# Performance work log

Hardware: AMD Instinct MI355X
Metric: run time of the kernel (lower is better)

Reference implementation:

```python
import jax, jax.numpy as jnp
import numpy as np

EMBED = 1024
HEADS = 16
HEAD_DIM = EMBED // HEADS


def setup_inputs() -> dict:
    key = jax.random.key(0)
    ks = jax.random.split(key, 8)
    B, S = 2, 2048
    value = jax.random.normal(ks[0], (B, S, EMBED), dtype=jnp.float32)
    key_t = jax.random.normal(ks[1], (B, S, EMBED), dtype=jnp.float32)
    query = jax.random.normal(ks[2], (B, S, EMBED), dtype=jnp.float32)
    scale = 1.0 / np.sqrt(EMBED)
    Wv = jax.random.normal(ks[3], (EMBED, EMBED), dtype=jnp.float32) * scale
    Wk = jax.random.normal(ks[4], (EMBED, EMBED), dtype=jnp.float32) * scale
    Wq = jax.random.normal(ks[5], (EMBED, EMBED), dtype=jnp.float32) * scale
    Wo = jax.random.normal(ks[6], (EMBED, EMBED), dtype=jnp.float32) * scale
    bo = jax.random.normal(ks[7], (EMBED,), dtype=jnp.float32) * 0.01
    return {"value": value, "key": key_t, "query": query,
            "Wv": Wv, "Wk": Wk, "Wq": Wq, "Wo": Wo, "bo": bo}


def reference(value, key, query, Wv, Wk, Wq, Wo, bo):
    B = query.shape[0]
    # Linear (torch: y = x @ W.T), then split heads -> [B, H, S, D]
    def split(x, W):
        y = jnp.einsum('bse,fe->bsf', x, W)
        return y.reshape(B, -1, HEADS, HEAD_DIM).transpose(0, 2, 1, 3)
    v = split(value, Wv)
    k = split(key, Wk)
    q = split(query, Wq)
    scores = jnp.einsum('bhqd,bhkd->bhqk', q, k) / jnp.sqrt(jnp.float32(HEAD_DIM))
    attn = jax.nn.softmax(scores, axis=-1)
    out = jnp.einsum('bhqk,bhkd->bhqd', attn, v)
    out = out.transpose(0, 2, 1, 3).reshape(B, -1, EMBED)
    return jnp.einsum('bse,fe->bsf', out, Wo) + bo
```

## Files before the change

kernel.cpp:

```cpp
#include <hip/hip_runtime.h>


#define SEQ   2048
#define EMB   1024
#define NHEAD 16
#define HDIM  64
#define NTOK  4096

typedef __attribute__((ext_vector_type(8))) __bf16 bf16x8;
typedef __attribute__((ext_vector_type(4))) float  f32x4;

#define OFF_XV  0u
#define OFF_XK  4194304u
#define OFF_XQ  8388608u
#define OFF_WV  12582912u
#define OFF_WK  13631488u
#define OFF_WQ  14680064u
#define OFF_WO  15728640u
#define OFF_VB  16777216u
#define OFF_KB  20971520u
#define OFF_QB  25165824u
#define OFF_VT  4194304u
#define OFF_ATT 0u

typedef __attribute__((address_space(1))) void g_void;
typedef __attribute__((address_space(3))) void l_void;

__device__ __forceinline__ void async_cp16(const void* g, void* l) {
  __builtin_amdgcn_global_load_lds((g_void*)(void*)g, (l_void*)l, 16, 0, 0);
}

__device__ __forceinline__ unsigned short f2bf(float f) {
  __bf16 h = (__bf16)f;
  return __builtin_bit_cast(unsigned short, h);
}

__device__ __forceinline__ f32x4 mfma16(bf16x8 a, bf16x8 b, f32x4 c) {
  return __builtin_amdgcn_mfma_f32_16x16x32_bf16(a, b, c, 0, 0, 0);
}

__global__ __launch_bounds__(256) void cvt_bf16(
    const float* __restrict__ s0, const float* __restrict__ s1,
    const float* __restrict__ s2, const float* __restrict__ s3,
    const float* __restrict__ s4, const float* __restrict__ s5,
    const float* __restrict__ s6, unsigned short* __restrict__ ws)
{
  int t = blockIdx.y;
  const float* s; unsigned off; int n8;
  switch (t) {
    case 0:  s = s0; off = OFF_XV; n8 = 524288; break;
    case 1:  s = s1; off = OFF_XK; n8 = 524288; break;
    case 2:  s = s2; off = OFF_XQ; n8 = 524288; break;
    case 3:  s = s3; off = OFF_WV; n8 = 131072; break;
    case 4:  s = s4; off = OFF_WK; n8 = 131072; break;
    case 5:  s = s5; off = OFF_WQ; n8 = 131072; break;
    default: s = s6; off = OFF_WO; n8 = 131072; break;
  }
  const float4* sf = (const float4*)s;
  unsigned short* d = ws + off;
  for (int i = blockIdx.x * 256 + threadIdx.x; i < n8; i += gridDim.x * 256) {
    float4 a = sf[2 * i], b = sf[2 * i + 1];
    uint4 o;
    o.x = (unsigned)f2bf(a.x) | ((unsigned)f2bf(a.y) << 16);
    o.y = (unsigned)f2bf(a.z) | ((unsigned)f2bf(a.w) << 16);
    o.z = (unsigned)f2bf(b.x) | ((unsigned)f2bf(b.y) << 16);
    o.w = (unsigned)f2bf(b.z) | ((unsigned)f2bf(b.w) << 16);
    *(uint4*)&d[(size_t)i * 8] = o;
  }
}

__global__ __launch_bounds__(256) void gemm_bf16(
    unsigned short* __restrict__ ws, float* __restrict__ dout,
    const float* __restrict__ bo, int mode_base)
{
  int mode = mode_base + blockIdx.z;
  const unsigned short* A;
  const unsigned short* W;
  if (mode == 0)      { A = ws + OFF_XV;  W = ws + OFF_WV; }
  else if (mode == 1) { A = ws + OFF_XK;  W = ws + OFF_WK; }
  else if (mode == 2) { A = ws + OFF_XQ;  W = ws + OFF_WQ; }
  else                { A = ws + OFF_ATT; W = ws + OFF_WO; }

  int tid = threadIdx.x;
  int lane = tid & 63;
  int wid = tid >> 6;
  int l15 = lane & 15, lg = lane >> 4;
  int wm = wid >> 1, wn = wid & 1;
  int m0 = blockIdx.y * 128, n0 = blockIdx.x * 128;
  int c0 = wid * 2;

  __shared__ unsigned short Ab[2][4096];
  __shared__ unsigned short Bb[2][4096];

  f32x4 acc[4][4];
#pragma unroll
  for (int i = 0; i < 4; ++i)
#pragma unroll
    for (int j = 0; j < 4; ++j) acc[i][j] = (f32x4)0.0f;

#pragma unroll
  for (int i = 0; i < 2; ++i) {
    int c = (c0 + i) * 64 + lane;
    int row = c >> 2, cs = c & 3;
    int sc = (cs ^ ((row >> 1) & 3)) * 8;
    async_cp16(A + (size_t)(m0 + row) * 1024 + sc, &Ab[0][(c0 + i) * 512]);
    async_cp16(W + (size_t)(n0 + row) * 1024 + sc, &Bb[0][(c0 + i) * 512]);
  }
  __syncthreads();

  for (int kt = 0; kt < 32; ++kt) {
    int cur = kt & 1;
    if (kt < 31) {
      int k0 = (kt + 1) * 32;
#pragma unroll
      for (int i = 0; i < 2; ++i) {
        int c = (c0 + i) * 64 + lane;
        int row = c >> 2, cs = c & 3;
        int sc = (cs ^ ((row >> 1) & 3)) * 8;
        async_cp16(A + (size_t)(m0 + row) * 1024 + k0 + sc, &Ab[cur ^ 1][(c0 + i) * 512]);
        async_cp16(W + (size_t)(n0 + row) * 1024 + k0 + sc, &Bb[cur ^ 1][(c0 + i) * 512]);
      }
    }
    bf16x8 af[4], bfr[4];
#pragma unroll
    for (int mf = 0; mf < 4; ++mf) {
      int ar = wm * 64 + mf * 16 + l15;
      af[mf] = *(const bf16x8*)&Ab[cur][ar * 32 + (lg ^ ((ar >> 1) & 3)) * 8];
    }
#pragma unroll
    for (int nf = 0; nf < 4; ++nf) {
      int br = wn * 64 + nf * 16 + l15;
      bfr[nf] = *(const bf16x8*)&Bb[cur][br * 32 + (lg ^ ((br >> 1) & 3)) * 8];
    }
#pragma unroll
    for (int mf = 0; mf < 4; ++mf)
#pragma unroll
      for (int nf = 0; nf < 4; ++nf)
        acc[mf][nf] = mfma16(af[mf], bfr[nf], acc[mf][nf]);
    __syncthreads();
  }

  if (mode < 3) {
    unsigned short* outp = ws + OFF_VB + (unsigned)mode * 4194304u;
    float scale = (mode == 2) ? 0.18033688011112042f : 1.0f;
#pragma unroll
    for (int mf = 0; mf < 4; ++mf)
#pragma unroll
      for (int nf = 0; nf < 4; ++nf)
#pragma unroll
        for (int r = 0; r < 4; ++r) {
          int token = m0 + wm * 64 + mf * 16 + lg * 4 + r;
          int col   = n0 + wn * 64 + nf * 16 + l15;
          size_t o = (((size_t)(token >> 11) * NHEAD + (col >> 6)) * SEQ
                      + (token & 2047)) * HDIM + (col & 63);
          outp[o] = f2bf(acc[mf][nf][r] * scale);
        }
  } else {
#pragma unroll
    for (int nf = 0; nf < 4; ++nf) {
      int col = n0 + wn * 64 + nf * 16 + l15;
      float bias = bo[col];
#pragma unroll
      for (int mf = 0; mf < 4; ++mf)
#pragma unroll
        for (int r = 0; r < 4; ++r) {
          int token = m0 + wm * 64 + mf * 16 + lg * 4 + r;
          dout[(size_t)token * EMB + col] = acc[mf][nf][r] + bias;
        }
    }
  }
}

__global__ __launch_bounds__(256) void vtrans(
    const unsigned short* __restrict__ vsrc, unsigned short* __restrict__ vdst)
{
  __shared__ unsigned short T[64][72];
  int tid = threadIdx.x;
  int bh = blockIdx.y;
  int s0 = blockIdx.x * 64;
  const unsigned short* v = vsrc + (size_t)bh * SEQ * HDIM;
  unsigned short* o = vdst + (size_t)bh * HDIM * SEQ;

  int r = tid >> 2, cq = tid & 3;
  const uint4* src = (const uint4*)&v[(size_t)(s0 + r) * HDIM + cq * 16];
  uint4 d0 = src[0], d1 = src[1];
  *(uint4*)&T[r][cq * 16]     = d0;
  *(uint4*)&T[r][cq * 16 + 8] = d1;
  __syncthreads();

  int d = tid >> 2, sc = tid & 3;
  uint4 t4[2];
  unsigned short* tmp = (unsigned short*)t4;
#pragma unroll
  for (int j = 0; j < 16; ++j) tmp[j] = T[sc * 16 + j][d];
  *(uint4*)&o[(size_t)d * SEQ + s0 + sc * 16]     = t4[0];
  *(uint4*)&o[(size_t)d * SEQ + s0 + sc * 16 + 8] = t4[1];
}

__global__ __launch_bounds__(256) void attn_fwd(unsigned short* __restrict__ ws)
{
  int tid = threadIdx.x, lane = tid & 63, wid = tid >> 6;
  int l15 = lane & 15, lg = lane >> 4;
  int bh = blockIdx.x & 31;
  int q0 = (blockIdx.x >> 5) * 128;

  const unsigned short* qb = ws + OFF_QB + (size_t)bh * SEQ * HDIM;
  const unsigned short* kb = ws + OFF_KB + (size_t)bh * SEQ * HDIM;
  const unsigned short* vt = ws + OFF_VT + (size_t)bh * HDIM * SEQ;
  unsigned short* att = ws + OFF_ATT;

  __shared__ unsigned short Kb[2][4096];
  __shared__ unsigned short Vb[2][4096];
  __shared__ unsigned short Pb[4][2304];

  bf16x8 qf[2][2];
#pragma unroll
  for (int mf = 0; mf < 2; ++mf)
#pragma unroll
    for (int kk = 0; kk < 2; ++kk)
      qf[mf][kk] = *(const bf16x8*)
          &qb[(size_t)(q0 + wid * 32 + mf * 16 + l15) * HDIM + kk * 32 + lg * 8];

  f32x4 O[2][4];
#pragma unroll
  for (int mf = 0; mf < 2; ++mf)
#pragma unroll
    for (int nf = 0; nf < 4; ++nf) O[mf][nf] = (f32x4)0.0f;
  float mrow[2][4], lp[2][4];
#pragma unroll
  for (int mf = 0; mf < 2; ++mf)
#pragma unroll
    for (int r = 0; r < 4; ++r) { mrow[mf][r] = -1e30f; lp[mf][r] = 0.0f; }

  int c0 = wid * 2;
  auto stage = [&](int buf, int kv0) {
#pragma unroll
    for (int i = 0; i < 2; ++i) {
      int c = (c0 + i) * 64 + lane;
      int row = c >> 3, cs = c & 7;
      int scol = (cs ^ (row & 7)) * 8;
      async_cp16(kb + (size_t)(kv0 + row) * HDIM + scol, &Kb[buf][(c0 + i) * 512]);
      async_cp16(vt + (size_t)row * SEQ + kv0 + scol,     &Vb[buf][(c0 + i) * 512]);
    }
  };

  stage(0, 0);
  __syncthreads();

  for (int it = 0; it < 32; ++it) {
    int cur = it & 1;
    if (it < 31) stage(cur ^ 1, (it + 1) * 64);

    f32x4 S[2][4];
#pragma unroll
    for (int mf = 0; mf < 2; ++mf)
#pragma unroll
      for (int nf = 0; nf < 4; ++nf) S[mf][nf] = (f32x4)0.0f;
#pragma unroll
    for (int kk = 0; kk < 2; ++kk) {
#pragma unroll
      for (int nf = 0; nf < 4; ++nf) {
        int row = nf * 16 + l15;
        int off = (row * 128 + kk * 64 + lg * 16) ^ ((row & 7) << 4);
        bf16x8 kf = *(const bf16x8*)((const char*)&Kb[cur][0] + off);
        S[0][nf] = mfma16(qf[0][kk], kf, S[0][nf]);
        S[1][nf] = mfma16(qf[1][kk], kf, S[1][nf]);
      }
    }

    float lmax[2][4];
    bool need = false;
#pragma unroll
    for (int mf = 0; mf < 2; ++mf)
#pragma unroll
      for (int r = 0; r < 4; ++r) {
        float rx = fmaxf(fmaxf(S[mf][0][r], S[mf][1][r]),
                         fmaxf(S[mf][2][r], S[mf][3][r]));
        lmax[mf][r] = rx;
        need = need || (rx > mrow[mf][r] + 8.0f);
      }
    if (__any((int)need)) {
#pragma unroll
      for (int mf = 0; mf < 2; ++mf)
#pragma unroll
        for (int r = 0; r < 4; ++r) {
          float rx = lmax[mf][r];
          rx = fmaxf(rx, __shfl_xor(rx, 1));
          rx = fmaxf(rx, __shfl_xor(rx, 2));
          rx = fmaxf(rx, __shfl_xor(rx, 4));
          rx = fmaxf(rx, __shfl_xor(rx, 8));
          float mold = mrow[mf][r];
          float mnew = fmaxf(mold, rx);
          float scl = __builtin_amdgcn_exp2f(mold - mnew);
          mrow[mf][r] = mnew;
          lp[mf][r] *= scl;
#pragma unroll
          for (int nf = 0; nf < 4; ++nf) O[mf][nf][r] *= scl;
        }
    }
#pragma unroll
    for (int mf = 0; mf < 2; ++mf)
#pragma unroll
      for (int r = 0; r < 4; ++r) {
        float m = mrow[mf][r];
        float s0 = __builtin_amdgcn_exp2f(S[mf][0][r] - m);
        float s1 = __builtin_amdgcn_exp2f(S[mf][1][r] - m);
        float s2 = __builtin_amdgcn_exp2f(S[mf][2][r] - m);
        float s3 = __builtin_amdgcn_exp2f(S[mf][3][r] - m);
        S[mf][0][r] = s0; S[mf][1][r] = s1; S[mf][2][r] = s2; S[mf][3][r] = s3;
        lp[mf][r] += (s0 + s1) + (s2 + s3);
      }

    unsigned short* pw = &Pb[wid][0];
#pragma unroll
    for (int mf = 0; mf < 2; ++mf)
#pragma unroll
      for (int nf = 0; nf < 4; ++nf)
#pragma unroll
        for (int r = 0; r < 4; ++r)
          pw[(mf * 16 + lg * 4 + r) * 72 + nf * 16 + l15] = f2bf(S[mf][nf][r]);

#pragma unroll
    for (int kk = 0; kk < 2; ++kk) {
      bf16x8 pf[2];
      pf[0] = *(const bf16x8*)&pw[(l15) * 72 + kk * 32 + lg * 8];
      pf[1] = *(const bf16x8*)&pw[(16 + l15) * 72 + kk * 32 + lg * 8];
#pragma unroll
      for (int nf = 0; nf < 4; ++nf) {
        int d = nf * 16 + l15;
        int off = (d * 128 + kk * 64 + lg * 16) ^ ((d & 7) << 4);
        bf16x8 vf = *(const bf16x8*)((const char*)&Vb[cur][0] + off);
        O[0][nf] = mfma16(pf[0], vf, O[0][nf]);
        O[1][nf] = mfma16(pf[1], vf, O[1][nf]);
      }
    }
    __syncthreads();
  }

  int b = bh >> 4, h = bh & 15;
#pragma unroll
  for (int mf = 0; mf < 2; ++mf)
#pragma unroll
    for (int r = 0; r < 4; ++r) {
      float ps = lp[mf][r];
      ps += __shfl_xor(ps, 1);
      ps += __shfl_xor(ps, 2);
      ps += __shfl_xor(ps, 4);
      ps += __shfl_xor(ps, 8);
      float inv = 1.0f / ps;
      int srow = q0 + wid * 32 + mf * 16 + lg * 4 + r;
#pragma unroll
      for (int nf = 0; nf < 4; ++nf) {
        int e = h * 64 + nf * 16 + l15;
        att[((size_t)b * SEQ + srow) * EMB + e] = f2bf(O[mf][nf][r] * inv);
      }
    }
}

extern "C" void kernel_launch(void* const* d_in, const int* in_sizes, int n_in,
                              void* d_out, int out_size, void* d_ws, size_t ws_size,
                              hipStream_t stream)
{
  const float* value = (const float*)d_in[0];
  const float* key_t = (const float*)d_in[1];
  const float* query = (const float*)d_in[2];
  const float* Wv = (const float*)d_in[3];
  const float* Wk = (const float*)d_in[4];
  const float* Wq = (const float*)d_in[5];
  const float* Wo = (const float*)d_in[6];
  const float* bo = (const float*)d_in[7];
  unsigned short* ws = (unsigned short*)d_ws;
  float* out = (float*)d_out;

  cvt_bf16<<<dim3(512, 7), 256, 0, stream>>>(value, key_t, query, Wv, Wk, Wq, Wo, ws);
  gemm_bf16<<<dim3(8, 32, 3), 256, 0, stream>>>(ws, out, bo, 0);
  vtrans<<<dim3(32, 32), 256, 0, stream>>>(ws + OFF_VB, ws + OFF_VT);
  attn_fwd<<<512, 256, 0, stream>>>(ws);
  gemm_bf16<<<dim3(8, 32, 1), 256, 0, stream>>>(ws, out, bo, 3);
}
```

Measured before the change: 263.2 us.

## Halve attention query tile per block, swizzle P buffer, add MFMA priority hints

The attention kernel now handles 64 query rows per block (16 per wave) instead of 128 and launches twice as many blocks, which cuts registers per wave and should raise occupancy and spread work across more CUs. The P staging buffer in LDS now uses an XOR-swizzled 64-wide layout instead of a padded 72-wide one, and s_setprio raises wave priority around the MFMA sections. The cost is that each K/V tile loaded into LDS is reused by half as many query rows, which doubles K/V global and LDS traffic per output row.

New measurement: 278.9 us. +6.0%, slower.

```diff
diff --git a/kernel.cpp b/kernel.cpp
--- a/kernel.cpp
+++ b/kernel.cpp
@@ -202,7 +202,7 @@
   int tid = threadIdx.x, lane = tid & 63, wid = tid >> 6;
   int l15 = lane & 15, lg = lane >> 4;
   int bh = blockIdx.x & 31;
-  int q0 = (blockIdx.x >> 5) * 128;
+  int q0 = (blockIdx.x >> 5) * 64;
 
   const unsigned short* qb = ws + OFF_QB + (size_t)bh * SEQ * HDIM;
   const unsigned short* kb = ws + OFF_KB + (size_t)bh * SEQ * HDIM;
@@ -211,26 +211,20 @@
 
   __shared__ unsigned short Kb[2][4096];
   __shared__ unsigned short Vb[2][4096];
-  __shared__ unsigned short Pb[4][2304];
-
-  bf16x8 qf[2][2];
-#pragma unroll
-  for (int mf = 0; mf < 2; ++mf)
-#pragma unroll
-    for (int kk = 0; kk < 2; ++kk)
-      qf[mf][kk] = *(const bf16x8*)
-          &qb[(size_t)(q0 + wid * 32 + mf * 16 + l15) * HDIM + kk * 32 + lg * 8];
-
-  f32x4 O[2][4];
-#pragma unroll
-  for (int mf = 0; mf < 2; ++mf)
-#pragma unroll
-    for (int nf = 0; nf < 4; ++nf) O[mf][nf] = (f32x4)0.0f;
-  float mrow[2][4], lp[2][4];
-#pragma unroll
-  for (int mf = 0; mf < 2; ++mf)
-#pragma unroll
-    for (int r = 0; r < 4; ++r) { mrow[mf][r] = -1e30f; lp[mf][r] = 0.0f; }
+  __shared__ unsigned short Pb[4][1024];
+
+  bf16x8 qf[2];
+#pragma unroll
+  for (int kk = 0; kk < 2; ++kk)
+    qf[kk] = *(const bf16x8*)
+        &qb[(size_t)(q0 + wid * 16 + l15) * HDIM + kk * 32 + lg * 8];
+
+  f32x4 O[4];
+#pragma unroll
+  for (int nf = 0; nf < 4; ++nf) O[nf] = (f32x4)0.0f;
+  float mrow[4], lp[4];
+#pragma unroll
+  for (int r = 0; r < 4; ++r) { mrow[r] = -1e30f; lp[r] = 0.0f; }
 
   int c0 = wid * 2;
   auto stage = [&](int buf, int kv0) {
@@ -251,11 +245,10 @@
     int cur = it & 1;
     if (it < 31) stage(cur ^ 1, (it + 1) * 64);
 
-    f32x4 S[2][4];
-#pragma unroll
-    for (int mf = 0; mf < 2; ++mf)
-#pragma unroll
-      for (int nf = 0; nf < 4; ++nf) S[mf][nf] = (f32x4)0.0f;
+    f32x4 S[4];
+#pragma unroll
+    for (int nf = 0; nf < 4; ++nf) S[nf] = (f32x4)0.0f;
+    __builtin_amdgcn_s_setprio(1);
 #pragma unroll
     for (int kk = 0; kk < 2; ++kk) {
 #pragma unroll
@@ -263,98 +256,90 @@
         int row = nf * 16 + l15;
         int off = (row * 128 + kk * 64 + lg * 16) ^ ((row & 7) << 4);
         bf16x8 kf = *(const bf16x8*)((const char*)&Kb[cur][0] + off);
-        S[0][nf] = mfma16(qf[0][kk], kf, S[0][nf]);
-        S[1][nf] = mfma16(qf[1][kk], kf, S[1][nf]);
-      }
-    }
-
-    float lmax[2][4];
+        S[nf] = mfma16(qf[kk], kf, S[nf]);
+      }
+    }
+    __builtin_amdgcn_s_setprio(0);
+
+    float lmax[4];
     bool need = false;
 #pragma unroll
-    for (int mf = 0; mf < 2; ++mf)
+    for (int r = 0; r < 4; ++r) {
+      float rx = fmaxf(fmaxf(S[0][r], S[1][r]), fmaxf(S[2][r], S[3][r]));
+      lmax[r] = rx;
+      need = need || (rx > mrow[r] + 8.0f);
+    }
+    if (__any((int)need)) {
 #pragma unroll
       for (int r = 0; r < 4; ++r) {
-        float rx = fmaxf(fmaxf(S[mf][0][r], S[mf][1][r]),
-                         fmaxf(S[mf][2][r], S[mf][3][r]));
-        lmax[mf][r] = rx;
-        need = need || (rx > mrow[mf][r] + 8.0f);
-      }
-    if (__any((int)need)) {
-#pragma unroll
-      for (int mf = 0; mf < 2; ++mf)
-#pragma unroll
-        for (int r = 0; r < 4; ++r) {
-          float rx = lmax[mf][r];
-          rx = fmaxf(rx, __shfl_xor(rx, 1));
-          rx = fmaxf(rx, __shfl_xor(rx, 2));
-          rx = fmaxf(rx, __shfl_xor(rx, 4));
-          rx = fmaxf(rx, __shfl_xor(rx, 8));
-          float mold = mrow[mf][r];
-          float mnew = fmaxf(mold, rx);
-          float scl = __builtin_amdgcn_exp2f(mold - mnew);
-          mrow[mf][r] = mnew;
-          lp[mf][r] *= scl;
-#pragma unroll
-          for (int nf = 0; nf < 4; ++nf) O[mf][nf][r] *= scl;
-        }
-    }
-#pragma unroll
-    for (int mf = 0; mf < 2; ++mf)
+        float rx = lmax[r];
+        rx = fmaxf(rx, __shfl_xor(rx, 1));
+        rx = fmaxf(rx, __shfl_xor(rx, 2));
+        rx = fmaxf(rx, __shfl_xor(rx, 4));
+        rx = fmaxf(rx, __shfl_xor(rx, 8));
+        float mold = mrow[r];
+        float mnew = fmaxf(mold, rx);
+        float scl = __builtin_amdgcn_exp2f(mold - mnew);
+        mrow[r] = mnew;
+        lp[r] *= scl;
+#pragma unroll
+        for (int nf = 0; nf < 4; ++nf) O[nf][r] *= scl;
+      }
+    }
+#pragma unroll
+    for (int r = 0; r < 4; ++r) {
+      float m = mrow[r];
+      float s0 = __builtin_amdgcn_exp2f(S[0][r] - m);
+      float s1 = __builtin_amdgcn_exp2f(S[1][r] - m);
+      float s2 = __builtin_amdgcn_exp2f(S[2][r] - m);
+      float s3 = __builtin_amdgcn_exp2f(S[3][r] - m);
+      S[0][r] = s0; S[1][r] = s1; S[2][r] = s2; S[3][r] = s3;
+      lp[r] += (s0 + s1) + (s2 + s3);
+    }
+
+    unsigned short* pw = &Pb[wid][0];
+#pragma unroll
+    for (int nf = 0; nf < 4; ++nf)
 #pragma unroll
       for (int r = 0; r < 4; ++r) {
-        float m = mrow[mf][r];
-        float s0 = __builtin_amdgcn_exp2f(S[mf][0][r] - m);
-        float s1 = __builtin_amdgcn_exp2f(S[mf][1][r] - m);
-        float s2 = __builtin_amdgcn_exp2f(S[mf][2][r] - m);
-        float s3 = __builtin_amdgcn_exp2f(S[mf][3][r] - m);
-        S[mf][0][r] = s0; S[mf][1][r] = s1; S[mf][2][r] = s2; S[mf][3][r] = s3;
-        lp[mf][r] += (s0 + s1) + (s2 + s3);
-      }
-
-    unsigned short* pw = &Pb[wid][0];
-#pragma unroll
-    for (int mf = 0; mf < 2; ++mf)
-#pragma unroll
-      for (int nf = 0; nf < 4; ++nf)
-#pragma unroll
-        for (int r = 0; r < 4; ++r)
-          pw[(mf * 16 + lg * 4 + r) * 72 + nf * 16 + l15] = f2bf(S[mf][nf][r]);
-
+        int m = lg * 4 + r;
+        int chunk = (nf * 2 + (l15 >> 3)) ^ (m & 7);
+        pw[m * 64 + chunk * 8 + (l15 & 7)] = f2bf(S[nf][r]);
+      }
+
+    __builtin_amdgcn_s_setprio(1);
 #pragma unroll
     for (int kk = 0; kk < 2; ++kk) {
-      bf16x8 pf[2];
-      pf[0] = *(const bf16x8*)&pw[(l15) * 72 + kk * 32 + lg * 8];
-      pf[1] = *(const bf16x8*)&pw[(16 + l15) * 72 + kk * 32 + lg * 8];
+      int chunk = (kk * 4 + lg) ^ (l15 & 7);
+      bf16x8 pf = *(const bf16x8*)&pw[l15 * 64 + chunk * 8];
 #pragma unroll
       for (int nf = 0; nf < 4; ++nf) {
         int d = nf * 16 + l15;
         int off = (d * 128 + kk * 64 + lg * 16) ^ ((d & 7) << 4);
         bf16x8 vf = *(const bf16x8*)((const char*)&Vb[cur][0] + off);
-        O[0][nf] = mfma16(pf[0], vf, O[0][nf]);
-        O[1][nf] = mfma16(pf[1], vf, O[1][nf]);
-      }
-    }
+        O[nf] = mfma16(pf, vf, O[nf]);
+      }
+    }
+    __builtin_amdgcn_s_setprio(0);
     __syncthreads();
   }
 
   int b = bh >> 4, h = bh & 15;
 #pragma unroll
-  for (int mf = 0; mf < 2; ++mf)
-#pragma unroll
-    for (int r = 0; r < 4; ++r) {
-      float ps = lp[mf][r];
-      ps += __shfl_xor(ps, 1);
-      ps += __shfl_xor(ps, 2);
-      ps += __shfl_xor(ps, 4);
-      ps += __shfl_xor(ps, 8);
-      float inv = 1.0f / ps;
-      int srow = q0 + wid * 32 + mf * 16 + lg * 4 + r;
-#pragma unroll
-      for (int nf = 0; nf < 4; ++nf) {
-        int e = h * 64 + nf * 16 + l15;
-        att[((size_t)b * SEQ + srow) * EMB + e] = f2bf(O[mf][nf][r] * inv);
-      }
-    }
+  for (int r = 0; r < 4; ++r) {
+    float ps = lp[r];
+    ps += __shfl_xor(ps, 1);
+    ps += __shfl_xor(ps, 2);
+    ps += __shfl_xor(ps, 4);
+    ps += __shfl_xor(ps, 8);
+    float inv = 1.0f / ps;
+    int srow = q0 + wid * 16 + lg * 4 + r;
+#pragma unroll
+    for (int nf = 0; nf < 4; ++nf) {
+      int e = h * 64 + nf * 16 + l15;
+      att[((size_t)b * SEQ + srow) * EMB + e] = f2bf(O[nf][r] * inv);
+    }
+  }
 }
 
 extern "C" void kernel_launch(void* const* d_in, const int* in_sizes, int n_in,
@@ -375,6 +360,6 @@
   cvt_bf16<<<dim3(512, 7), 256, 0, stream>>>(value, key_t, query, Wv, Wk, Wq, Wo, ws);
   gemm_bf16<<<dim3(8, 32, 3), 256, 0, stream>>>(ws, out, bo, 0);
   vtrans<<<dim3(32, 32), 256, 0, stream>>>(ws + OFF_VB, ws + OFF_VT);
-  attn_fwd<<<512, 256, 0, stream>>>(ws);
+  attn_fwd<<<1024, 256, 0, stream>>>(ws);
   gemm_bf16<<<dim3(8, 32, 1), 256, 0, stream>>>(ws, out, bo, 3);
 }
```

## Fuse V transpose into projection GEMM and keep attention P in registers

Applied to the files above, without the earlier changes.

The projection GEMM epilogue now stages results through shared memory and writes coalesced 16-byte stores. For V it writes the transposed [d, s] layout directly, which removes the separate vtrans kernel and its extra pass over V. The attention kernel computes S transposed (K as the A operand, with a permuted K row order) so each lane holds a full query row. This lets P be packed into bf16 MFMA operands in registers without an LDS round-trip, and it simplifies the row max and sum reductions. s_setprio hints are also added around the MFMA blocks; the main risk is the correctness of the permutation and layout mapping.

Result: faster. 219.8 us (-16.5%).

```diff
diff --git a/kernel.cpp b/kernel.cpp
--- a/kernel.cpp
+++ b/kernel.cpp
@@ -17,10 +17,9 @@
 #define OFF_WK  13631488u
 #define OFF_WQ  14680064u
 #define OFF_WO  15728640u
-#define OFF_VB  16777216u
+#define OFF_VT  16777216u
 #define OFF_KB  20971520u
 #define OFF_QB  25165824u
-#define OFF_VT  4194304u
 #define OFF_ATT 0u
 
 typedef __attribute__((address_space(1))) void g_void;
@@ -89,8 +88,9 @@
   int m0 = blockIdx.y * 128, n0 = blockIdx.x * 128;
   int c0 = wid * 2;
 
-  __shared__ unsigned short Ab[2][4096];
-  __shared__ unsigned short Bb[2][4096];
+  __shared__ unsigned short SM[16384];
+  unsigned short (*Ab)[4096] = (unsigned short(*)[4096])SM;
+  unsigned short (*Bb)[4096] = (unsigned short(*)[4096])(SM + 8192);
 
   f32x4 acc[4][4];
 #pragma unroll
@@ -132,16 +132,40 @@
       int br = wn * 64 + nf * 16 + l15;
       bfr[nf] = *(const bf16x8*)&Bb[cur][br * 32 + (lg ^ ((br >> 1) & 3)) * 8];
     }
+    __builtin_amdgcn_s_setprio(1);
 #pragma unroll
     for (int mf = 0; mf < 4; ++mf)
 #pragma unroll
       for (int nf = 0; nf < 4; ++nf)
         acc[mf][nf] = mfma16(af[mf], bfr[nf], acc[mf][nf]);
+    __builtin_amdgcn_s_setprio(0);
     __syncthreads();
   }
 
-  if (mode < 3) {
-    unsigned short* outp = ws + OFF_VB + (unsigned)mode * 4194304u;
+  if (mode == 0) {
+#pragma unroll
+    for (int mf = 0; mf < 4; ++mf)
+#pragma unroll
+      for (int nf = 0; nf < 4; ++nf)
+#pragma unroll
+        for (int r = 0; r < 4; ++r) {
+          int c = wn * 64 + nf * 16 + l15;
+          int s = wm * 64 + mf * 16 + lg * 4 + r;
+          SM[c * 128 + (s ^ ((c & 7) << 3))] = f2bf(acc[mf][nf][r]);
+        }
+    __syncthreads();
+    int sidx = tid & 15, cbase = tid >> 4;
+    size_t b = (size_t)(m0 >> 11);
+#pragma unroll
+    for (int i = 0; i < 8; ++i) {
+      int c = i * 16 + cbase;
+      int h = (n0 >> 6) + (c >> 6);
+      uint4 v = *(const uint4*)&SM[c * 128 + ((sidx ^ (c & 7)) * 8)];
+      size_t bh = b * NHEAD + h;
+      *(uint4*)&ws[OFF_VT + (bh * HDIM + (c & 63)) * SEQ + (m0 & 2047) + sidx * 8] = v;
+    }
+  } else if (mode < 3) {
+    unsigned short* outp = ws + ((mode == 1) ? OFF_KB : OFF_QB);
     float scale = (mode == 2) ? 0.18033688011112042f : 1.0f;
 #pragma unroll
     for (int mf = 0; mf < 4; ++mf)
@@ -149,12 +173,22 @@
       for (int nf = 0; nf < 4; ++nf)
 #pragma unroll
         for (int r = 0; r < 4; ++r) {
-          int token = m0 + wm * 64 + mf * 16 + lg * 4 + r;
-          int col   = n0 + wn * 64 + nf * 16 + l15;
-          size_t o = (((size_t)(token >> 11) * NHEAD + (col >> 6)) * SEQ
-                      + (token & 2047)) * HDIM + (col & 63);
-          outp[o] = f2bf(acc[mf][nf][r] * scale);
-        }
+          int s = wm * 64 + mf * 16 + lg * 4 + r;
+          int c = wn * 64 + nf * 16 + l15;
+          SM[s * 128 + (c ^ ((s & 7) << 3))] = f2bf(acc[mf][nf][r] * scale);
+        }
+    __syncthreads();
+    int l = tid & 15, rb = tid >> 4;
+    int half = l >> 3, j = l & 7;
+    size_t b = (size_t)(m0 >> 11);
+#pragma unroll
+    for (int i = 0; i < 8; ++i) {
+      int s = i * 16 + rb;
+      uint4 v = *(const uint4*)&SM[s * 128 + half * 64 + ((j ^ (s & 7)) * 8)];
+      int h = (n0 >> 6) + half;
+      size_t bh = b * NHEAD + h;
+      *(uint4*)&outp[(bh * SEQ + ((m0 + s) & 2047)) * HDIM + j * 8] = v;
+    }
   } else {
 #pragma unroll
     for (int nf = 0; nf < 4; ++nf) {
@@ -169,32 +203,6 @@
         }
     }
   }
-}
-
-__global__ __launch_bounds__(256) void vtrans(
-    const unsigned short* __restrict__ vsrc, unsigned short* __restrict__ vdst)
-{
-  __shared__ unsigned short T[64][72];
-  int tid = threadIdx.x;
-  int bh = blockIdx.y;
-  int s0 = blockIdx.x * 64;
-  const unsigned short* v = vsrc + (size_t)bh * SEQ * HDIM;
-  unsigned short* o = vdst + (size_t)bh * HDIM * SEQ;
-
-  int r = tid >> 2, cq = tid & 3;
-  const uint4* src = (const uint4*)&v[(size_t)(s0 + r) * HDIM + cq * 16];
-  uint4 d0 = src[0], d1 = src[1];
-  *(uint4*)&T[r][cq * 16]     = d0;
-  *(uint4*)&T[r][cq * 16 + 8] = d1;
-  __syncthreads();
-
-  int d = tid >> 2, sc = tid & 3;
-  uint4 t4[2];
-  unsigned short* tmp = (unsigned short*)t4;
-#pragma unroll
-  for (int j = 0; j < 16; ++j) tmp[j] = T[sc * 16 + j][d];
-  *(uint4*)&o[(size_t)d * SEQ + s0 + sc * 16]     = t4[0];
-  *(uint4*)&o[(size_t)d * SEQ + s0 + sc * 16 + 8] = t4[1];
 }
 
 __global__ __launch_bounds__(256) void attn_fwd(unsigned short* __restrict__ ws)
@@ -211,7 +219,6 @@
 
   __shared__ unsigned short Kb[2][4096];
   __shared__ unsigned short Vb[2][4096];
-  __shared__ unsigned short Pb[4][2304];
 
   bf16x8 qf[2][2];
 #pragma unroll
@@ -226,21 +233,20 @@
   for (int mf = 0; mf < 2; ++mf)
 #pragma unroll
     for (int nf = 0; nf < 4; ++nf) O[mf][nf] = (f32x4)0.0f;
-  float mrow[2][4], lp[2][4];
-#pragma unroll
-  for (int mf = 0; mf < 2; ++mf)
-#pragma unroll
-    for (int r = 0; r < 4; ++r) { mrow[mf][r] = -1e30f; lp[mf][r] = 0.0f; }
+  float mrow[2], lp[2];
+#pragma unroll
+  for (int mf = 0; mf < 2; ++mf) { mrow[mf] = -1e30f; lp[mf] = 0.0f; }
 
   int c0 = wid * 2;
   auto stage = [&](int buf, int kv0) {
 #pragma unroll
     for (int i = 0; i < 2; ++i) {
       int c = (c0 + i) * 64 + lane;
-      int row = c >> 3, cs = c & 7;
-      int scol = (cs ^ (row & 7)) * 8;
-      async_cp16(kb + (size_t)(kv0 + row) * HDIM + scol, &Kb[buf][(c0 + i) * 512]);
-      async_cp16(vt + (size_t)row * SEQ + kv0 + scol,     &Vb[buf][(c0 + i) * 512]);
+      int p = c >> 3, cs = c & 7;
+      int scol = (cs ^ (p & 7)) * 8;
+      int kpi = ((p >> 4) & 1) * 32 + ((p >> 2) & 3) * 8 + (p >> 5) * 4 + (p & 3);
+      async_cp16(kb + (size_t)(kv0 + kpi) * HDIM + scol, &Kb[buf][(c0 + i) * 512]);
+      async_cp16(vt + (size_t)p * SEQ + kv0 + scol,       &Vb[buf][(c0 + i) * 512]);
     }
   };
 
@@ -256,98 +262,107 @@
     for (int mf = 0; mf < 2; ++mf)
 #pragma unroll
       for (int nf = 0; nf < 4; ++nf) S[mf][nf] = (f32x4)0.0f;
+    __builtin_amdgcn_s_setprio(1);
 #pragma unroll
     for (int kk = 0; kk < 2; ++kk) {
 #pragma unroll
       for (int nf = 0; nf < 4; ++nf) {
-        int row = nf * 16 + l15;
-        int off = (row * 128 + kk * 64 + lg * 16) ^ ((row & 7) << 4);
+        int p = nf * 16 + l15;
+        int off = (p * 128 + kk * 64 + lg * 16) ^ ((p & 7) << 4);
         bf16x8 kf = *(const bf16x8*)((const char*)&Kb[cur][0] + off);
-        S[0][nf] = mfma16(qf[0][kk], kf, S[0][nf]);
-        S[1][nf] = mfma16(qf[1][kk], kf, S[1][nf]);
-      }
-    }
-
-    float lmax[2][4];
+        S[0][nf] = mfma16(kf, qf[0][kk], S[0][nf]);
+        S[1][nf] = mfma16(kf, qf[1][kk], S[1][nf]);
+      }
+    }
+    __builtin_amdgcn_s_setprio(0);
+
+    float lmax[2];
     bool need = false;
 #pragma unroll
-    for (int mf = 0; mf < 2; ++mf)
-#pragma unroll
-      for (int r = 0; r < 4; ++r) {
-        float rx = fmaxf(fmaxf(S[mf][0][r], S[mf][1][r]),
-                         fmaxf(S[mf][2][r], S[mf][3][r]));
-        lmax[mf][r] = rx;
-        need = need || (rx > mrow[mf][r] + 8.0f);
-      }
+    for (int mf = 0; mf < 2; ++mf) {
+      float rx = S[mf][0][0];
+#pragma unroll
+      for (int nf = 0; nf < 4; ++nf)
+#pragma unroll
+        for (int r = 0; r < 4; ++r) rx = fmaxf(rx, S[mf][nf][r]);
+      lmax[mf] = rx;
+      need = need || (rx > mrow[mf] + 8.0f);
+    }
     if (__any((int)need)) {
+      float scl[2];
+#pragma unroll
+      for (int mf = 0; mf < 2; ++mf) {
+        float rx = lmax[mf];
+        rx = fmaxf(rx, __shfl_xor(rx, 16));
+        rx = fmaxf(rx, __shfl_xor(rx, 32));
+        float mold = mrow[mf];
+        float mnew = fmaxf(mold, rx);
+        scl[mf] = __builtin_amdgcn_exp2f(mold - mnew);
+        mrow[mf] = mnew;
+        lp[mf] *= scl[mf];
+      }
 #pragma unroll
       for (int mf = 0; mf < 2; ++mf)
 #pragma unroll
         for (int r = 0; r < 4; ++r) {
-          float rx = lmax[mf][r];
-          rx = fmaxf(rx, __shfl_xor(rx, 1));
-          rx = fmaxf(rx, __shfl_xor(rx, 2));
-          rx = fmaxf(rx, __shfl_xor(rx, 4));
-          rx = fmaxf(rx, __shfl_xor(rx, 8));
-          float mold = mrow[mf][r];
-          float mnew = fmaxf(mold, rx);
-          float scl = __builtin_amdgcn_exp2f(mold - mnew);
-          mrow[mf][r] = mnew;
-          lp[mf][r] *= scl;
-#pragma unroll
-          for (int nf = 0; nf < 4; ++nf) O[mf][nf][r] *= scl;
-        }
-    }
-#pragma unroll
-    for (int mf = 0; mf < 2; ++mf)
-#pragma unroll
-      for (int r = 0; r < 4; ++r) {
-        float m = mrow[mf][r];
-        float s0 = __builtin_amdgcn_exp2f(S[mf][0][r] - m);
-        float s1 = __builtin_amdgcn_exp2f(S[mf][1][r] - m);
-        float s2 = __builtin_amdgcn_exp2f(S[mf][2][r] - m);
-        float s3 = __builtin_amdgcn_exp2f(S[mf][3][r] - m);
-        S[mf][0][r] = s0; S[mf][1][r] = s1; S[mf][2][r] = s2; S[mf][3][r] = s3;
-        lp[mf][r] += (s0 + s1) + (s2 + s3);
-      }
-
-    unsigned short* pw = &Pb[wid][0];
-#pragma unroll
-    for (int mf = 0; mf < 2; ++mf)
-#pragma unroll
-      for (int nf = 0; nf < 4; ++nf)
-#pragma unroll
-        for (int r = 0; r < 4; ++r)
-          pw[(mf * 16 + lg * 4 + r) * 72 + nf * 16 + l15] = f2bf(S[mf][nf][r]);
-
+          float f = __shfl(scl[mf], lg * 4 + r);
+#pragma unroll
+          for (int nf = 0; nf < 4; ++nf) O[mf][nf][r] *= f;
+        }
+    }
+#pragma unroll
+    for (int mf = 0; mf < 2; ++mf) {
+      float m = mrow[mf];
+      float acc0 = 0.0f, acc1 = 0.0f;
+#pragma unroll
+      for (int nf = 0; nf < 4; ++nf)
+#pragma unroll
+        for (int r = 0; r < 4; ++r) {
+          float e = __builtin_amdgcn_exp2f(S[mf][nf][r] - m);
+          S[mf][nf][r] = e;
+          if (r & 1) acc1 += e; else acc0 += e;
+        }
+      lp[mf] += acc0 + acc1;
+    }
+
+    __builtin_amdgcn_s_setprio(1);
 #pragma unroll
     for (int kk = 0; kk < 2; ++kk) {
-      bf16x8 pf[2];
-      pf[0] = *(const bf16x8*)&pw[(l15) * 72 + kk * 32 + lg * 8];
-      pf[1] = *(const bf16x8*)&pw[(16 + l15) * 72 + kk * 32 + lg * 8];
+      bf16x8 pa[2];
+#pragma unroll
+      for (int mf = 0; mf < 2; ++mf)
+#pragma unroll
+        for (int j = 0; j < 4; ++j) {
+          pa[mf][j]     = (__bf16)S[mf][kk][j];
+          pa[mf][4 + j] = (__bf16)S[mf][2 + kk][j];
+        }
 #pragma unroll
       for (int nf = 0; nf < 4; ++nf) {
         int d = nf * 16 + l15;
         int off = (d * 128 + kk * 64 + lg * 16) ^ ((d & 7) << 4);
         bf16x8 vf = *(const bf16x8*)((const char*)&Vb[cur][0] + off);
-        O[0][nf] = mfma16(pf[0], vf, O[0][nf]);
-        O[1][nf] = mfma16(pf[1], vf, O[1][nf]);
-      }
-    }
+        O[0][nf] = mfma16(pa[0], vf, O[0][nf]);
+        O[1][nf] = mfma16(pa[1], vf, O[1][nf]);
+      }
+    }
+    __builtin_amdgcn_s_setprio(0);
     __syncthreads();
   }
 
   int b = bh >> 4, h = bh & 15;
+  float lr[2];
+#pragma unroll
+  for (int mf = 0; mf < 2; ++mf) {
+    float s = lp[mf];
+    s += __shfl_xor(s, 16);
+    s += __shfl_xor(s, 32);
+    lr[mf] = s;
+  }
 #pragma unroll
   for (int mf = 0; mf < 2; ++mf)
 #pragma unroll
     for (int r = 0; r < 4; ++r) {
-      float ps = lp[mf][r];
-      ps += __shfl_xor(ps, 1);
-      ps += __shfl_xor(ps, 2);
-      ps += __shfl_xor(ps, 4);
-      ps += __shfl_xor(ps, 8);
-      float inv = 1.0f / ps;
+      float inv = 1.0f / __shfl(lr[mf], lg * 4 + r);
       int srow = q0 + wid * 32 + mf * 16 + lg * 4 + r;
 #pragma unroll
       for (int nf = 0; nf < 4; ++nf) {
@@ -374,7 +389,6 @@
 
   cvt_bf16<<<dim3(512, 7), 256, 0, stream>>>(value, key_t, query, Wv, Wk, Wq, Wo, ws);
   gemm_bf16<<<dim3(8, 32, 3), 256, 0, stream>>>(ws, out, bo, 0);
-  vtrans<<<dim3(32, 32), 256, 0, stream>>>(ws + OFF_VB, ws + OFF_VT);
   attn_fwd<<<512, 256, 0, stream>>>(ws);
   gemm_bf16<<<dim3(8, 32, 1), 256, 0, stream>>>(ws, out, bo, 3);
 }
```
